# Kernel tuning notes

Measured on AMD Instinct MI355X. Metric: run time of the kernel, lower is better.

The kernel has to match this reference:

```python
import jax, jax.numpy as jnp
import numpy as np


def setup_inputs() -> dict:
    key = jax.random.key(0)
    ks = jax.random.split(key, 8)
    B, N, M = 8, 4096, 4096
    return {
        "R": jax.random.normal(ks[0], (B, 3, 3), dtype=jnp.float32),
        "t": jax.random.normal(ks[1], (B, 3), dtype=jnp.float32),
        "S": jax.random.uniform(ks[2], (B,), dtype=jnp.float32),
        "R_g": jax.random.normal(ks[3], (B, 3, 3), dtype=jnp.float32),
        "t_g": jax.random.normal(ks[4], (B, 3), dtype=jnp.float32),
        "S_g": jax.random.uniform(ks[5], (B,), dtype=jnp.float32),
        "T_X": jax.random.normal(ks[6], (B, N, 3), dtype=jnp.float32),
        "Y": jax.random.normal(ks[7], (B, M, 3), dtype=jnp.float32),
    }


def _chamfer(x, y):
    # x: [B,N,3], y: [B,M,3]. Pairwise Euclidean distances [B,N,M] via the
    x2 = jnp.sum(x * x, axis=-1)                      # [B,N]
    y2 = jnp.sum(y * y, axis=-1)                      # [B,M]
    xy = jnp.einsum('bnd,bmd->bnm', x, y)             # [B,N,M]
    d2 = x2[:, :, None] + y2[:, None, :] - 2.0 * xy
    dist = jnp.sqrt(jnp.maximum(d2, 0.0))             # [B,N,M]
    min_x_to_y = jnp.min(dist, axis=2)                # [B,N]
    min_y_to_x = jnp.min(dist, axis=1)                # [B,M]
    per_batch = jnp.mean(min_x_to_y, axis=1) + jnp.mean(min_y_to_x, axis=1)
    return jnp.mean(per_batch)


def _registration(R, t, S, R_g, t_g, S_g):
    eye = jnp.eye(3, dtype=R.dtype)
    diff = jnp.einsum('bji,bjk->bik', R_g, R) - eye   # R_g^T @ R - I, [B,3,3]
    L_R = jnp.sum(diff * diff, axis=(1, 2))           # squared Frobenius norm
    L_t = jnp.sum((t_g - t) ** 2, axis=1)
    L_S = (S_g - S) ** 2
    return jnp.mean(L_R + L_t + L_S)


def reference(R, t, S, R_g, t_g, S_g, T_X, Y):
    L_R = _registration(R, t, S, R_g, t_g, S_g)
    L_CD = _chamfer(T_X, Y)
    return (L_R + L_CD, L_R, L_CD)
```

## Files before the change

### kernel.cpp

```cpp
#include <hip/hip_runtime.h>
#include <hip/hip_bf16.h>

constexpr int B_ = 8;
constexpr int N_ = 4096;
constexpr int M_ = 4096;
constexpr int TPB1 = 1024;
constexpr int QPB = 256;
constexpr int QUARTER = M_ / 4;
constexpr int NTILE = QUARTER / 16;
constexpr int NBLK = 2 * B_ * (N_ / QPB);

typedef _Float16 half8 __attribute__((ext_vector_type(8)));
typedef float    f32x4 __attribute__((ext_vector_type(4)));

__global__ __launch_bounds__(TPB1) void chamfer_fused(
    const float* __restrict__ X, const float* __restrict__ Yp,
    float* __restrict__ part)
{
    __shared__ half8 sB[M_ + 1];
    __shared__ float smin[4 * QPB];
    __shared__ float wsum16[16];

    int bid = blockIdx.x;
    const int dir    = bid & 1;   bid >>= 1;
    const int qchunk = bid & 15;  bid >>= 4;
    const int b      = bid;

    const float* q  = dir ? Yp : X;
    const float* db = dir ? X  : Yp;

    const int tid  = threadIdx.x;
    const int lane = tid & 63;
    const int wave = tid >> 6;
    const int quarter = wave & 3;
    const int qgroup  = wave >> 2;
    const int l15  = lane & 15;

    const int dbbase = b * M_;
    #pragma unroll
    for (int k = 0; k < M_ / TPB1; ++k) {
        const int pt = tid + k * TPB1;
        const float* pp = db + (size_t)(dbbase + pt) * 3;
        float px = pp[0], py = pp[1], pz = pp[2];
        float pn = px * px + py * py + pz * pz;
        half8 v;
        v[0] = (_Float16)(-2.0f * px);
        v[1] = (_Float16)(-2.0f * py);
        v[2] = (_Float16)(-2.0f * pz);
        v[3] = (_Float16)pn;
        v[4] = (_Float16)0.0f; v[5] = (_Float16)0.0f;
        v[6] = (_Float16)0.0f; v[7] = (_Float16)0.0f;
        sB[pt] = v;
    }
    if (tid == 0) {
        half8 z;
        #pragma unroll
        for (int i = 0; i < 8; ++i) z[i] = (_Float16)0.0f;
        sB[M_] = z;
    }

    const int qglob = b * N_ + qchunk * QPB + qgroup * 64;
    half8 af[4];
    #pragma unroll
    for (int f = 0; f < 4; ++f) {
        half8 v;
        #pragma unroll
        for (int i = 0; i < 8; ++i) v[i] = (_Float16)0.0f;
        if (lane < 16) {
            const float* qp = q + (size_t)(qglob + f * 16 + l15) * 3;
            v[0] = (_Float16)qp[0];
            v[1] = (_Float16)qp[1];
            v[2] = (_Float16)qp[2];
            v[3] = (_Float16)1.0f;
        }
        af[f] = v;
    }
    __syncthreads();

    const half8* bp = sB + ((lane < 16) ? (quarter * QUARTER + l15) : M_);
    const int step  = (lane < 16) ? 16 : 0;

    f32x4 zero4; zero4[0] = 0.f; zero4[1] = 0.f; zero4[2] = 0.f; zero4[3] = 0.f;
    const float BIG = 3.0e38f;
    float rm[4][4];
    #pragma unroll
    for (int f = 0; f < 4; ++f)
        #pragma unroll
        for (int i = 0; i < 4; ++i) rm[f][i] = BIG;

    for (int t = 0; t < NTILE; t += 2) {
        half8 b0 = bp[0];
        half8 b1 = bp[step];
        bp += (step << 1);
        f32x4 a0[4], a1[4];
        #pragma unroll
        for (int f = 0; f < 4; ++f)
            a0[f] = __builtin_amdgcn_mfma_f32_16x16x32_f16(af[f], b0, zero4, 0, 0, 0);
        #pragma unroll
        for (int f = 0; f < 4; ++f)
            a1[f] = __builtin_amdgcn_mfma_f32_16x16x32_f16(af[f], b1, zero4, 0, 0, 0);
        #pragma unroll
        for (int f = 0; f < 4; ++f)
            #pragma unroll
            for (int i = 0; i < 4; ++i)
                rm[f][i] = fminf(rm[f][i], fminf(a0[f][i], a1[f][i]));
    }

    #pragma unroll
    for (int f = 0; f < 4; ++f)
        #pragma unroll
        for (int i = 0; i < 4; ++i) {
            float v = rm[f][i];
            v = fminf(v, __shfl_xor(v, 1, 64));
            v = fminf(v, __shfl_xor(v, 2, 64));
            v = fminf(v, __shfl_xor(v, 4, 64));
            v = fminf(v, __shfl_xor(v, 8, 64));
            rm[f][i] = v;
        }

    const int f_sel = (lane >> 2) & 3;
    const int i_sel = lane & 3;
    float v = BIG;
    #pragma unroll
    for (int f = 0; f < 4; ++f)
        #pragma unroll
        for (int i = 0; i < 4; ++i)
            if (f == f_sel && i == i_sel) v = rm[f][i];

    const int j = f_sel * 16 + ((lane >> 4) << 2) + i_sel;
    smin[quarter * QPB + qgroup * 64 + j] = v;
    __syncthreads();

    float d = 0.0f;
    if (tid < QPB) {
        float m = fminf(fminf(smin[tid], smin[QPB + tid]),
                        fminf(smin[2 * QPB + tid], smin[3 * QPB + tid]));
        const float* qp = q + (size_t)(b * N_ + qchunk * QPB + tid) * 3;
        const float qn = qp[0] * qp[0] + qp[1] * qp[1] + qp[2] * qp[2];
        d = sqrtf(fmaxf(m + qn, 0.0f));
    }
    #pragma unroll
    for (int off = 32; off > 0; off >>= 1) d += __shfl_down(d, off, 64);
    if (lane == 0) wsum16[wave] = d;
    __syncthreads();
    if (tid == 0) {
        float s = 0.0f;
        #pragma unroll
        for (int w = 0; w < 16; ++w) s += wsum16[w];
        part[blockIdx.x] = s;
    }
}

__global__ __launch_bounds__(256) void final_kernel(
    const float* __restrict__ part,
    const float* __restrict__ R,  const float* __restrict__ t,
    const float* __restrict__ S,  const float* __restrict__ Rg,
    const float* __restrict__ tg, const float* __restrict__ Sg,
    float* __restrict__ out)
{
    __shared__ float wsum[4];
    __shared__ float sreg[8];
    const int tid = threadIdx.x;

    float s = part[tid];
    #pragma unroll
    for (int off = 32; off > 0; off >>= 1) s += __shfl_down(s, off, 64);
    if ((tid & 63) == 0) wsum[tid >> 6] = s;

    if (tid < 8) {
        const float* Rb  = R  + tid * 9;
        const float* Rgb = Rg + tid * 9;
        float acc = 0.0f;
        #pragma unroll
        for (int i = 0; i < 3; ++i) {
            #pragma unroll
            for (int k = 0; k < 3; ++k) {
                float v = 0.0f;
                #pragma unroll
                for (int jj = 0; jj < 3; ++jj)
                    v = fmaf(Rgb[jj * 3 + i], Rb[jj * 3 + k], v);
                if (i == k) v -= 1.0f;
                acc = fmaf(v, v, acc);
            }
        }
        #pragma unroll
        for (int dd = 0; dd < 3; ++dd) {
            float dv = tg[tid * 3 + dd] - t[tid * 3 + dd];
            acc = fmaf(dv, dv, acc);
        }
        float dS = Sg[tid] - S[tid];
        acc = fmaf(dS, dS, acc);
        sreg[tid] = acc;
    }
    __syncthreads();

    if (tid == 0) {
        float tot = wsum[0] + wsum[1] + wsum[2] + wsum[3];
        float L_CD = tot / (float)(B_ * N_);
        float rs = 0.0f;
        #pragma unroll
        for (int bb = 0; bb < 8; ++bb) rs += sreg[bb];
        float L_R = rs / (float)B_;
        out[0] = L_R + L_CD;
        out[1] = L_R;
        out[2] = L_CD;
    }
}

extern "C" void kernel_launch(void* const* d_in, const int* in_sizes, int n_in,
                              void* d_out, int out_size, void* d_ws, size_t ws_size,
                              hipStream_t stream) {
    const float* R  = (const float*)d_in[0];
    const float* t  = (const float*)d_in[1];
    const float* S  = (const float*)d_in[2];
    const float* Rg = (const float*)d_in[3];
    const float* tg = (const float*)d_in[4];
    const float* Sg = (const float*)d_in[5];
    const float* X  = (const float*)d_in[6];
    const float* Yp = (const float*)d_in[7];
    float* out = (float*)d_out;

    float* part = (float*)d_ws;

    chamfer_fused<<<NBLK, TPB1, 0, stream>>>(X, Yp, part);
    final_kernel<<<1, 256, 0, stream>>>(part, R, t, S, Rg, tg, Sg, out);
}
```

Before: 82.40 us.

## Fuse final reduction into chamfer kernel via last-block atomic counter and vectorize loads

Drops the separate final_kernel launch. Each block now bumps a global atomic counter after writing its partial, and the last block to finish reduces all partials and computes the registration loss. The database point load is also rewritten to use three float4 loads per thread instead of scalar strided loads. This adds a hipMemsetAsync launch to reset the counter, plus threadfence and atomic overhead in every block.

```diff
diff --git a/kernel.cpp b/kernel.cpp
--- a/kernel.cpp
+++ b/kernel.cpp
@@ -13,13 +13,19 @@
 typedef _Float16 half8 __attribute__((ext_vector_type(8)));
 typedef float    f32x4 __attribute__((ext_vector_type(4)));
 
-__global__ __launch_bounds__(TPB1) void chamfer_fused(
+__global__ __launch_bounds__(TPB1) void chamfer_all(
     const float* __restrict__ X, const float* __restrict__ Yp,
-    float* __restrict__ part)
+    const float* __restrict__ R,  const float* __restrict__ t,
+    const float* __restrict__ S,  const float* __restrict__ Rg,
+    const float* __restrict__ tg, const float* __restrict__ Sg,
+    float* __restrict__ part, int* __restrict__ counter,
+    float* __restrict__ out)
 {
     __shared__ half8 sB[M_ + 1];
     __shared__ float smin[4 * QPB];
     __shared__ float wsum16[16];
+    __shared__ float sreg[8];
+    __shared__ int   sflag;
 
     int bid = blockIdx.x;
     const int dir    = bid & 1;   bid >>= 1;
@@ -36,21 +42,26 @@
     const int qgroup  = wave >> 2;
     const int l15  = lane & 15;
 
-    const int dbbase = b * M_;
-    #pragma unroll
-    for (int k = 0; k < M_ / TPB1; ++k) {
-        const int pt = tid + k * TPB1;
-        const float* pp = db + (size_t)(dbbase + pt) * 3;
-        float px = pp[0], py = pp[1], pz = pp[2];
-        float pn = px * px + py * py + pz * pz;
-        half8 v;
-        v[0] = (_Float16)(-2.0f * px);
-        v[1] = (_Float16)(-2.0f * py);
-        v[2] = (_Float16)(-2.0f * pz);
-        v[3] = (_Float16)pn;
-        v[4] = (_Float16)0.0f; v[5] = (_Float16)0.0f;
-        v[6] = (_Float16)0.0f; v[7] = (_Float16)0.0f;
-        sB[pt] = v;
+    {
+        const float4* src4 = (const float4*)(db + (size_t)b * M_ * 3);
+        float4 f0 = src4[tid * 3 + 0];
+        float4 f1 = src4[tid * 3 + 1];
+        float4 f2 = src4[tid * 3 + 2];
+        float px[4] = {f0.x, f0.w, f1.z, f2.y};
+        float py[4] = {f0.y, f1.x, f1.w, f2.z};
+        float pz[4] = {f0.z, f1.y, f2.x, f2.w};
+        #pragma unroll
+        for (int i = 0; i < 4; ++i) {
+            float pn = px[i] * px[i] + py[i] * py[i] + pz[i] * pz[i];
+            half8 v;
+            v[0] = (_Float16)(-2.0f * px[i]);
+            v[1] = (_Float16)(-2.0f * py[i]);
+            v[2] = (_Float16)(-2.0f * pz[i]);
+            v[3] = (_Float16)pn;
+            v[4] = (_Float16)0.0f; v[5] = (_Float16)0.0f;
+            v[6] = (_Float16)0.0f; v[7] = (_Float16)0.0f;
+            sB[tid * 4 + i] = v;
+        }
     }
     if (tid == 0) {
         half8 z;
@@ -88,7 +99,7 @@
         #pragma unroll
         for (int i = 0; i < 4; ++i) rm[f][i] = BIG;
 
-    for (int t = 0; t < NTILE; t += 2) {
+    for (int tt = 0; tt < NTILE; tt += 2) {
         half8 b0 = bp[0];
         half8 b1 = bp[step];
         bp += (step << 1);
@@ -143,67 +154,63 @@
     for (int off = 32; off > 0; off >>= 1) d += __shfl_down(d, off, 64);
     if (lane == 0) wsum16[wave] = d;
     __syncthreads();
+
     if (tid == 0) {
         float s = 0.0f;
         #pragma unroll
         for (int w = 0; w < 16; ++w) s += wsum16[w];
         part[blockIdx.x] = s;
-    }
-}
-
-__global__ __launch_bounds__(256) void final_kernel(
-    const float* __restrict__ part,
-    const float* __restrict__ R,  const float* __restrict__ t,
-    const float* __restrict__ S,  const float* __restrict__ Rg,
-    const float* __restrict__ tg, const float* __restrict__ Sg,
-    float* __restrict__ out)
-{
-    __shared__ float wsum[4];
-    __shared__ float sreg[8];
-    const int tid = threadIdx.x;
-
-    float s = part[tid];
-    #pragma unroll
-    for (int off = 32; off > 0; off >>= 1) s += __shfl_down(s, off, 64);
-    if ((tid & 63) == 0) wsum[tid >> 6] = s;
-
-    if (tid < 8) {
-        const float* Rb  = R  + tid * 9;
-        const float* Rgb = Rg + tid * 9;
-        float acc = 0.0f;
-        #pragma unroll
-        for (int i = 0; i < 3; ++i) {
-            #pragma unroll
-            for (int k = 0; k < 3; ++k) {
-                float v = 0.0f;
+        __threadfence();
+        int old = atomicAdd(counter, 1);
+        sflag = (old == NBLK - 1) ? 1 : 0;
+    }
+    __syncthreads();
+
+    if (sflag) {
+        __threadfence();
+        if (tid < 8) {
+            const float* Rb  = R  + tid * 9;
+            const float* Rgb = Rg + tid * 9;
+            float acc = 0.0f;
+            #pragma unroll
+            for (int i = 0; i < 3; ++i) {
                 #pragma unroll
-                for (int jj = 0; jj < 3; ++jj)
-                    v = fmaf(Rgb[jj * 3 + i], Rb[jj * 3 + k], v);
-                if (i == k) v -= 1.0f;
-                acc = fmaf(v, v, acc);
+                for (int k = 0; k < 3; ++k) {
+                    float vv = 0.0f;
+                    #pragma unroll
+                    for (int jj = 0; jj < 3; ++jj)
+                        vv = fmaf(Rgb[jj * 3 + i], Rb[jj * 3 + k], vv);
+                    if (i == k) vv -= 1.0f;
+                    acc = fmaf(vv, vv, acc);
+                }
             }
-        }
-        #pragma unroll
-        for (int dd = 0; dd < 3; ++dd) {
-            float dv = tg[tid * 3 + dd] - t[tid * 3 + dd];
-            acc = fmaf(dv, dv, acc);
-        }
-        float dS = Sg[tid] - S[tid];
-        acc = fmaf(dS, dS, acc);
-        sreg[tid] = acc;
-    }
-    __syncthreads();
-
-    if (tid == 0) {
-        float tot = wsum[0] + wsum[1] + wsum[2] + wsum[3];
-        float L_CD = tot / (float)(B_ * N_);
-        float rs = 0.0f;
-        #pragma unroll
-        for (int bb = 0; bb < 8; ++bb) rs += sreg[bb];
-        float L_R = rs / (float)B_;
-        out[0] = L_R + L_CD;
-        out[1] = L_R;
-        out[2] = L_CD;
+            #pragma unroll
+            for (int dd = 0; dd < 3; ++dd) {
+                float dv = tg[tid * 3 + dd] - t[tid * 3 + dd];
+                acc = fmaf(dv, dv, acc);
+            }
+            float dS = Sg[tid] - S[tid];
+            acc = fmaf(dS, dS, acc);
+            sreg[tid] = acc;
+        }
+        float s = (tid < NBLK) ? ((volatile float*)part)[tid] : 0.0f;
+        #pragma unroll
+        for (int off = 32; off > 0; off >>= 1) s += __shfl_down(s, off, 64);
+        if (lane == 0) wsum16[wave] = s;
+        __syncthreads();
+        if (tid == 0) {
+            float tot = 0.0f;
+            #pragma unroll
+            for (int w = 0; w < 16; ++w) tot += wsum16[w];
+            float L_CD = tot / (float)(B_ * N_);
+            float rs = 0.0f;
+            #pragma unroll
+            for (int bb = 0; bb < 8; ++bb) rs += sreg[bb];
+            float L_R = rs / (float)B_;
+            out[0] = L_R + L_CD;
+            out[1] = L_R;
+            out[2] = L_CD;
+        }
     }
 }
 
@@ -220,8 +227,10 @@
     const float* Yp = (const float*)d_in[7];
     float* out = (float*)d_out;
 
-    float* part = (float*)d_ws;
-
-    chamfer_fused<<<NBLK, TPB1, 0, stream>>>(X, Yp, part);
-    final_kernel<<<1, 256, 0, stream>>>(part, R, t, S, Rg, tg, Sg, out);
+    float* part   = (float*)d_ws;
+    int* counter  = (int*)(part + NBLK);
+
+    hipMemsetAsync(counter, 0, sizeof(int), stream);
+    chamfer_all<<<NBLK, TPB1, 0, stream>>>(X, Yp, R, t, S, Rg, tg, Sg,
+                                           part, counter, out);
 }
```

Result: slower. 90.35 us (+9.7%).
